# Optimization experiments

Hardware: AMD Instinct MI355X
Metric: run time of the kernel (lower is better)

## Reference

```python
import jax, jax.numpy as jnp
import numpy as np

IM_H, IM_W = 128, 128       # im_size
HT_H, HT_W = 184, 180       # ht_size (rho x theta)
N_VOTES = 4_000_000         # number of (pixel, bin, weight) vote triples
NORM = float(max(IM_H, IM_W))


def setup_inputs() -> dict:
    key = jax.random.key(0)
    k1, k2, k3, k4 = jax.random.split(key, 4)
    x = jax.random.normal(k1, (2, 16, IM_H, IM_W), dtype=jnp.float32)
    vote_pixel = jax.random.randint(k2, (N_VOTES,), 0, IM_H * IM_W)   # pixel flat index
    vote_bin = jax.random.randint(k3, (N_VOTES,), 0, HT_H * HT_W)     # HT bin flat index
    vote_weight = jax.random.uniform(k4, (N_VOTES,), dtype=jnp.float32)
    return {"x": x, "vote_pixel": vote_pixel, "vote_bin": vote_bin,
            "vote_weight": vote_weight}


def reference(x, vote_pixel, vote_bin, vote_weight):
    # The original view(b*2, c//2, r, w) is a pure reshape; the scatter is
    # independent per (batch, channel) map, so we flatten all maps together.
    b, c, r, w = x.shape
    xf = x.reshape(b * c, r * w)                         # [BC, P]
    gathered = xf[:, vote_pixel] * vote_weight[None, :]  # [BC, N]
    # weighted scatter-add into HT bins (segment sum over leading axis)
    out = jax.ops.segment_sum(gathered.T, vote_bin, num_segments=HT_H * HT_W)  # [HB, BC]
    out = out.T.reshape(b, c, HT_H, HT_W)
    return out / NORM
```

## Files before the change

### kernel.cpp

```cpp
#include <hip/hip_runtime.h>
#include <stdint.h>

#define IM_HW   16384
#define NBINS   33120
#define NMAPS   32
#define INV_NORM (1.0f / 128.0f)

#define BBITS   5
#define NBUCK   1035
#define CAPB    4352
#define SLAB    192
#define SSTR    194
#define NB_SCAT 256
#define OVR_CAP 8192

__device__ __forceinline__ float w_from_top13(unsigned e) {
  const unsigned short hb = (unsigned short)((e >> 19) << 3);
  return (float)__builtin_bit_cast(_Float16, hb);
}

__global__ __launch_bounds__(1024) void k_scatter_bucket(
    const float* __restrict__ x, float* __restrict__ xT,
    const int* __restrict__ vp, const int* __restrict__ vb,
    const float* __restrict__ vw, int nv,
    unsigned* __restrict__ globcur,
    unsigned* __restrict__ ovrcnt,
    uint2*   __restrict__ ovrlist,
    unsigned* __restrict__ sorted) {
  __shared__ unsigned h[NBUCK];
  __shared__ unsigned lstart[NBUCK];
  __shared__ unsigned cur[NBUCK];
  __shared__ unsigned sc[1024];
  __shared__ unsigned lds[16384];

  const int tid = threadIdx.x;

  {
    const int base = blockIdx.x * 2048;
    #pragma unroll
    for (int k = 0; k < 2; ++k) {
      const int i = base + k * 1024 + tid;
      const int m = i & 31, p = i >> 5;
      xT[i] = x[m * IM_HW + p];
    }
  }

  const int chunk = (((nv + NB_SCAT - 1) / NB_SCAT) + 3) & ~3;
  const int c0 = blockIdx.x * chunk;
  const int c1 = min(nv, c0 + chunk);
  const int cnt = (c1 > c0) ? (c1 - c0) : 0;

  for (int i = tid; i < NBUCK; i += 1024) h[i] = 0u;
  __syncthreads();

  unsigned e[16];
  unsigned short rr[16], bu16[16];
  const int ng = cnt >> 2;
  const int4*   vp4 = (const int4*)(vp + c0);
  const int4*   vb4 = (const int4*)(vb + c0);
  const float4* vw4 = (const float4*)(vw + c0);
  #pragma unroll
  for (int j = 0; j < 4; ++j) {
    const int g = tid + j * 1024;
    if (g < ng) {
      const int4 p = vp4[g]; const int4 b = vb4[g]; const float4 w = vw4[g];
      const int k = j * 4;
      #define STAGE(q, PP, BB, WW) { \
        const unsigned short hw = __builtin_bit_cast(unsigned short, (_Float16)(WW)); \
        e[k + q] = (unsigned)(PP) | (((unsigned)(BB) & 31u) << 14) | (((unsigned)hw >> 3) << 19); \
        bu16[k + q] = (unsigned short)((unsigned)(BB) >> BBITS); \
        rr[k + q] = (unsigned short)atomicAdd(&h[(unsigned)(BB) >> BBITS], 1u); }
      STAGE(0, p.x, b.x, w.x) STAGE(1, p.y, b.y, w.y)
      STAGE(2, p.z, b.z, w.z) STAGE(3, p.w, b.w, w.w)
      #undef STAGE
    }
  }
  const int tail0 = ng * 4;
  if (tid < cnt - tail0) {
    const int gi = c0 + tail0 + tid;
    unsigned o = atomicAdd(ovrcnt, 1u);
    if (o < OVR_CAP)
      ovrlist[o] = make_uint2((unsigned)vp[gi] | ((unsigned)vb[gi] << 14),
                              __float_as_uint(vw[gi]));
  }
  __syncthreads();

  {
    const int i0 = 2 * tid, i1 = 2 * tid + 1;
    const unsigned a0 = (i0 < NBUCK) ? h[i0] : 0u;
    const unsigned a1 = (i1 < NBUCK) ? h[i1] : 0u;
    const unsigned s2 = a0 + a1;
    sc[tid] = s2;
    __syncthreads();
    for (int d = 1; d < 1024; d <<= 1) {
      const unsigned v = (tid >= d) ? sc[tid - d] : 0u;
      __syncthreads();
      sc[tid] += v;
      __syncthreads();
    }
    const unsigned base = sc[tid] - s2;
    if (i0 < NBUCK) lstart[i0] = base;
    if (i1 < NBUCK) lstart[i1] = base + a0;
  }
  for (int i = tid; i < NBUCK; i += 1024)
    cur[i] = (h[i] != 0u) ? atomicAdd(&globcur[i], h[i]) : 0u;
  __syncthreads();

  #pragma unroll
  for (int j = 0; j < 4; ++j) {
    const int g = tid + j * 1024;
    if (g < ng) {
      #pragma unroll
      for (int q = 0; q < 4; ++q) {
        const int k = j * 4 + q;
        lds[lstart[bu16[k]] + (unsigned)rr[k]] = e[k];
      }
    }
  }
  __syncthreads();

  const int wid = tid >> 6, lane = tid & 63;
  for (int bu = wid; bu < NBUCK; bu += 16) {
    const unsigned c = h[bu];
    if (c == 0u) continue;
    const unsigned gb = cur[bu], lb = lstart[bu];
    for (unsigned s = lane; s < c; s += 64) {
      const unsigned E = lds[lb + s];
      const unsigned g = gb + s;
      if (g < CAPB) {
        sorted[(size_t)bu * CAPB + g] = E;
      } else {
        unsigned o = atomicAdd(ovrcnt, 1u);
        if (o < OVR_CAP) {
          const unsigned pp  = E & 0x3FFFu;
          const unsigned bin = ((unsigned)bu << BBITS) + ((E >> 14) & 31u);
          ovrlist[o] = make_uint2(pp | (bin << 14), __float_as_uint(w_from_top13(E)));
        }
      }
    }
  }
}

__global__ __launch_bounds__(512) void k_spmm_static(
    const unsigned* __restrict__ sorted, const unsigned* __restrict__ globcur,
    const float* __restrict__ xT, float* __restrict__ out,
    unsigned* __restrict__ ovrcnt, uint2* __restrict__ ovrlist) {
  __shared__ unsigned sv[32 * SSTR];
  __shared__ unsigned cur[32];
  __shared__ float tile[32][33];
  const int tid = threadIdx.x;
  const int bu = blockIdx.x;
  const int n = min((int)globcur[bu], CAPB);

  if (tid < 32) cur[tid] = 0u;
  __syncthreads();

  const uint4* src = (const uint4*)(sorted + (size_t)bu * CAPB);
  const int nq = n >> 2;
  #define PLACE(E) { \
    const unsigned fb = ((E) >> 14) & 31u; \
    const unsigned s = atomicAdd(&cur[fb], 1u); \
    if (s < SLAB) sv[fb * SSTR + s] = (E) & 0xFFF83FFFu; \
    else { \
      unsigned o = atomicAdd(ovrcnt, 1u); \
      if (o < OVR_CAP) \
        ovrlist[o] = make_uint2(((E) & 0x3FFFu) | ((((unsigned)bu << BBITS) + fb) << 14), \
                                __float_as_uint(w_from_top13(E))); } }
  for (int i = tid; i < nq; i += 512) {
    const uint4 q = src[i];
    PLACE(q.x) PLACE(q.y) PLACE(q.z) PLACE(q.w)
  }
  if (tid < (n & 3)) {
    const unsigned E = sorted[(size_t)bu * CAPB + (n & ~3) + tid];
    PLACE(E)
  }
  #undef PLACE
  __syncthreads();

  #define WDEC(E) ((float)__builtin_bit_cast(_Float16, (unsigned short)((E) >> 16)))
  const int wv = tid >> 6, lane = tid & 63, half = lane >> 5, m = lane & 31;
  #pragma unroll
  for (int s4 = 0; s4 < 4; ++s4) {
    const int b = wv * 4 + s4;
    const int cnt = min((int)cur[b], SLAB);
    const unsigned* seg = &sv[b * SSTR];
    float acc = 0.0f;
    int base = 0;
    for (; base + 8 <= cnt; base += 8) {
      const uint2 a = *(const uint2*)(seg + base + 2 * half);
      const uint2 c = *(const uint2*)(seg + base + 4 + 2 * half);
      acc += WDEC(a.x) * xT[(a.x & 0x3FFFu) * 32 + m];
      acc += WDEC(a.y) * xT[(a.y & 0x3FFFu) * 32 + m];
      acc += WDEC(c.x) * xT[(c.x & 0x3FFFu) * 32 + m];
      acc += WDEC(c.y) * xT[(c.y & 0x3FFFu) * 32 + m];
    }
    for (; base + 4 <= cnt; base += 4) {
      const uint2 a = *(const uint2*)(seg + base + 2 * half);
      acc += WDEC(a.x) * xT[(a.x & 0x3FFFu) * 32 + m];
      acc += WDEC(a.y) * xT[(a.y & 0x3FFFu) * 32 + m];
    }
    if (half == 0) {
      for (int j = base; j < cnt; ++j) {
        const unsigned E = seg[j];
        acc += WDEC(E) * xT[(E & 0x3FFFu) * 32 + m];
      }
    }
    acc += __shfl_xor(acc, 32);
    if (lane < 32)
      tile[b][m] = acc * INV_NORM;
  }
  #undef WDEC
  __syncthreads();

  {
    const int row  = tid >> 4;
    const int col2 = (tid & 15) * 2;
    const int gb0  = bu << BBITS;
    const float2 v2 = make_float2(tile[col2][row], tile[col2 + 1][row]);
    *(float2*)(out + (size_t)row * NBINS + gb0 + col2) = v2;
  }
}

__global__ __launch_bounds__(1024) void k_overflow(
    const uint2* __restrict__ ovrlist, const unsigned* __restrict__ ovrcnt,
    const float* __restrict__ xT, float* __restrict__ out) {
  unsigned nz = *ovrcnt;
  unsigned n = nz < (unsigned)OVR_CAP ? nz : (unsigned)OVR_CAP;
  unsigned total = n * 32u;
  for (unsigned i = blockIdx.x * 1024u + threadIdx.x; i < total;
       i += gridDim.x * 1024u) {
    unsigned vi = i >> 5, m = i & 31u;
    uint2 vv = ovrlist[vi];
    unsigned p = vv.x & 0x3FFFu, bin = vv.x >> 14;
    atomicAdd(&out[(size_t)m * NBINS + bin],
              __uint_as_float(vv.y) * xT[p * 32 + m] * INV_NORM);
  }
}

__global__ __launch_bounds__(1024) void ht_fallback(const float* __restrict__ x,
                                                    const int* __restrict__ vp,
                                                    const int* __restrict__ vb,
                                                    const float* __restrict__ vw,
                                                    float* __restrict__ out, int nv) {
  __shared__ float hist[NBINS];
  for (int i = threadIdx.x; i < NBINS; i += 1024) hist[i] = 0.0f;
  __syncthreads();
  const int map = blockIdx.x >> 3, chunk = blockIdx.x & 7;
  const float* xm = x + map * IM_HW;
  const int per = (nv + 7) / 8;
  const int start = chunk * per, end = min(nv, start + per);
  for (int i = start + (int)threadIdx.x; i < end; i += 1024)
    atomicAdd(&hist[vb[i]], xm[vp[i]] * vw[i]);
  __syncthreads();
  float* om = out + map * NBINS;
  for (int i = threadIdx.x; i < NBINS; i += 1024)
    atomicAdd(&om[i], hist[i] * INV_NORM);
}

extern "C" void kernel_launch(void* const* d_in, const int* in_sizes, int n_in,
                              void* d_out, int out_size, void* d_ws, size_t ws_size,
                              hipStream_t stream) {
  const float* x  = (const float*)d_in[0];
  const int*   vp = (const int*)d_in[1];
  const int*   vb = (const int*)d_in[2];
  const float* vw = (const float*)d_in[3];
  float* out = (float*)d_out;
  const int nv = in_sizes[1];

  char* w = (char*)d_ws;
  unsigned* sorted  = (unsigned*)w; w += (size_t)NBUCK * CAPB * 4;
  float*    xT      = (float*)w;    w += (size_t)IM_HW * NMAPS * 4;
  uint2*    ovrlist = (uint2*)w;    w += (size_t)OVR_CAP * 8;
  unsigned* globcur = (unsigned*)w; w += (size_t)NBUCK * 4;
  unsigned* ovrcnt  = (unsigned*)w; w += 16;
  const size_t need = (size_t)(w - (char*)d_ws);

  if (ws_size >= need) {
    hipMemsetAsync(globcur, 0, (size_t)NBUCK * 4 + 16, stream);
    k_scatter_bucket<<<NB_SCAT, 1024, 0, stream>>>(x, xT, vp, vb, vw, nv, globcur,
                                                   ovrcnt, ovrlist, sorted);
    k_spmm_static<<<NBUCK, 512, 0, stream>>>(sorted, globcur, xT, out,
                                             ovrcnt, ovrlist);
    k_overflow<<<8, 1024, 0, stream>>>(ovrlist, ovrcnt, xT, out);
  } else {
    hipMemsetAsync(out, 0, (size_t)out_size * sizeof(float), stream);
    ht_fallback<<<256, 1024, 0, stream>>>(x, vp, vb, vw, out, nv);
  }
}
```

Before: 156.9 us.

## Replace block-wide scan with wavefront shuffle scan and fuse overflow into spmm

The 1024-thread LDS prefix scan over bucket counts, which needed about 20 barriers, is replaced by a single-wavefront scan: each of 64 lanes sums 17 buckets serially, then the lanes combine with shuffles. The separate overflow kernel is removed. Each spmm block now reads the overflow list and adds the entries that fall in its own bucket into the shared tile before the store. This saves a kernel launch and global atomics, but every block scans the whole overflow list, which costs extra when that list is non-empty.

```diff
diff --git a/kernel.cpp b/kernel.cpp
--- a/kernel.cpp
+++ b/kernel.cpp
@@ -30,7 +30,6 @@
   __shared__ unsigned h[NBUCK];
   __shared__ unsigned lstart[NBUCK];
   __shared__ unsigned cur[NBUCK];
-  __shared__ unsigned sc[1024];
   __shared__ unsigned lds[16384];
 
   const int tid = threadIdx.x;
@@ -85,23 +84,20 @@
   }
   __syncthreads();
 
-  {
-    const int i0 = 2 * tid, i1 = 2 * tid + 1;
-    const unsigned a0 = (i0 < NBUCK) ? h[i0] : 0u;
-    const unsigned a1 = (i1 < NBUCK) ? h[i1] : 0u;
-    const unsigned s2 = a0 + a1;
-    sc[tid] = s2;
-    __syncthreads();
-    for (int d = 1; d < 1024; d <<= 1) {
-      const unsigned v = (tid >= d) ? sc[tid - d] : 0u;
-      __syncthreads();
-      sc[tid] += v;
-      __syncthreads();
-    }
-    const unsigned base = sc[tid] - s2;
-    if (i0 < NBUCK) lstart[i0] = base;
-    if (i1 < NBUCK) lstart[i1] = base + a0;
-  }
+  if (tid < 64) {
+    const int lo = tid * 17, hi = min(NBUCK, lo + 17);
+    unsigned s = 0;
+    for (int i = lo; i < hi; ++i) s += h[i];
+    unsigned inc = s;
+    #pragma unroll
+    for (int d = 1; d < 64; d <<= 1) {
+      const unsigned v = __shfl_up(inc, d);
+      if (tid >= d) inc += v;
+    }
+    unsigned run = inc - s;
+    for (int i = lo; i < hi; ++i) { lstart[i] = run; run += h[i]; }
+  }
+  __syncthreads();
   for (int i = tid; i < NBUCK; i += 1024)
     cur[i] = (h[i] != 0u) ? atomicAdd(&globcur[i], h[i]) : 0u;
   __syncthreads();
@@ -213,27 +209,28 @@
   __syncthreads();
 
   {
+    unsigned nov = *ovrcnt;
+    nov = nov < (unsigned)OVR_CAP ? nov : (unsigned)OVR_CAP;
+    if (nov) {
+      for (unsigned idx = tid; idx < nov * 32u; idx += 512u) {
+        const unsigned vi = idx >> 5, m2 = idx & 31u;
+        const uint2 vv = ovrlist[vi];
+        const unsigned bin = vv.x >> 14;
+        if ((bin >> BBITS) == (unsigned)bu) {
+          atomicAdd(&tile[bin & 31u][m2],
+                    __uint_as_float(vv.y) * xT[(vv.x & 0x3FFFu) * 32 + m2] * INV_NORM);
+        }
+      }
+      __syncthreads();
+    }
+  }
+
+  {
     const int row  = tid >> 4;
     const int col2 = (tid & 15) * 2;
     const int gb0  = bu << BBITS;
     const float2 v2 = make_float2(tile[col2][row], tile[col2 + 1][row]);
     *(float2*)(out + (size_t)row * NBINS + gb0 + col2) = v2;
-  }
-}
-
-__global__ __launch_bounds__(1024) void k_overflow(
-    const uint2* __restrict__ ovrlist, const unsigned* __restrict__ ovrcnt,
-    const float* __restrict__ xT, float* __restrict__ out) {
-  unsigned nz = *ovrcnt;
-  unsigned n = nz < (unsigned)OVR_CAP ? nz : (unsigned)OVR_CAP;
-  unsigned total = n * 32u;
-  for (unsigned i = blockIdx.x * 1024u + threadIdx.x; i < total;
-       i += gridDim.x * 1024u) {
-    unsigned vi = i >> 5, m = i & 31u;
-    uint2 vv = ovrlist[vi];
-    unsigned p = vv.x & 0x3FFFu, bin = vv.x >> 14;
-    atomicAdd(&out[(size_t)m * NBINS + bin],
-              __uint_as_float(vv.y) * xT[p * 32 + m] * INV_NORM);
   }
 }
 
@@ -281,7 +278,6 @@
                                                    ovrcnt, ovrlist, sorted);
     k_spmm_static<<<NBUCK, 512, 0, stream>>>(sorted, globcur, xT, out,
                                              ovrcnt, ovrlist);
-    k_overflow<<<8, 1024, 0, stream>>>(ovrlist, ovrcnt, xT, out);
   } else {
     hipMemsetAsync(out, 0, (size_t)out_size * sizeof(float), stream);
     ht_fallback<<<256, 1024, 0, stream>>>(x, vp, vb, vw, out, nv);
```

Result: no change. 154.9 us (-1.3%).
